# Kernel tuning notes

Hardware: AMD Instinct MI355X
Metric: run time of the kernel (lower is better)

## Reference

```python
import jax, jax.numpy as jnp
import numpy as np
from jax import lax

RADIUS = 2
DILATION = 2

def _mind_kernels():
    # 6-neighbourhood offsets within a 3x3x3 stencil
    six = np.array([[0, 1, 1], [1, 1, 0], [1, 0, 1], [1, 1, 2], [2, 1, 1], [1, 2, 1]], dtype=np.int64)
    # pairwise squared distances between the 6 offsets
    dist = ((six[:, None, :] - six[None, :, :]) ** 2).sum(-1)  # [6,6]
    i, j = np.meshgrid(np.arange(6), np.arange(6), indexing='ij')
    mask = ((i > j) & (dist == 2)).ravel()  # 12 True entries
    idx1 = six[np.repeat(np.arange(6), 6)][mask]  # [12,3]
    idx2 = six[np.tile(np.arange(6), 6)][mask]    # [12,3]
    m1 = np.zeros((12, 1, 3, 3, 3), np.float32)
    m2 = np.zeros((12, 1, 3, 3, 3), np.float32)
    m1[np.arange(12), 0, idx1[:, 0], idx1[:, 1], idx1[:, 2]] = 1.0
    m2[np.arange(12), 0, idx2[:, 0], idx2[:, 1], idx2[:, 2]] = 1.0
    return jnp.asarray(m1), jnp.asarray(m2)

MSHIFT1, MSHIFT2 = _mind_kernels()

def _rep_pad(x, p):
    # ReplicationPad3d on NCDHW
    return jnp.pad(x, ((0, 0), (0, 0), (p, p), (p, p), (p, p)), mode='edge')

def _shift_conv(x, w):
    # Conv3d(1->12, k=3, stride=1, padding=1, dilation=DILATION, bias=False)
    return lax.conv_general_dilated(
        x, w, window_strides=(1, 1, 1),
        padding=((1, 1), (1, 1), (1, 1)),
        rhs_dilation=(DILATION, DILATION, DILATION),
        dimension_numbers=('NCDHW', 'OIDHW', 'NCDHW'))

def _avg_pool3d(x, k):
    s = lax.reduce_window(x, jnp.float32(0.0), lax.add,
                          (1, 1, k, k, k), (1, 1, 1, 1, 1), 'VALID')
    return s / jnp.float32(k ** 3)

def mind3d(x):
    xp = _rep_pad(x, DILATION)
    diff = _shift_conv(xp, MSHIFT1) - _shift_conv(xp, MSHIFT2)  # [B,12,D+2,H+2,W+2]
    ssd = _avg_pool3d(_rep_pad(diff * diff, RADIUS), 2 * RADIUS + 1)
    mind = ssd - jnp.min(ssd, axis=1, keepdims=True)
    mind_var = jnp.mean(mind, axis=1, keepdims=True)  # [B,1,...]
    mv_mean = jnp.mean(mind_var)
    mind_var = jnp.clip(mind_var, mv_mean * 0.001, mv_mean * 1000.0)
    return jnp.exp(-mind / mind_var)

def setup_inputs() -> dict:
    key = jax.random.key(0)
    x = jax.random.uniform(key, (1, 1, 128, 128, 128), dtype=jnp.float32)
    return {"x": x}

def reference(x):
    return mind3d(x)
```

## Files before the change

kernel.cpp:

```cpp
#include <hip/hip_runtime.h>
#include <math.h>

#define N    130
#define NN   (130*130)
#define NNN  (130*130*130)
#define NQ4  (NNN/4)
#define NCH  12
#define XN   128
#define XNN  (XN*XN)

#define WT   11
#define HT   11
#define DSEGS 13
#define NWG  (WT*HT*DSEGS)

typedef float f32x4 __attribute__((ext_vector_type(4)));

template <int CTRL>
__device__ __forceinline__ float dppf(float v) {
    return __int_as_float(__builtin_amdgcn_update_dpp(
        0, __float_as_int(v), CTRL, 0xF, 0xF, true));
}
#define W5(v) ((v) + dppf<0x111>(v) + dppf<0x112>(v) \
                   + dppf<0x101>(v) + dppf<0x102>(v))

__global__ __launch_bounds__(256) void k_fused(const float* __restrict__ x,
                                               float* __restrict__ Cout,
                                               float* __restrict__ MV,
                                               double* __restrict__ acc,
                                               unsigned* __restrict__ gmm) {
    const int tid = threadIdx.x;
    const int wl  = tid & 15;
    const int r   = tid >> 4;

    const int qq  = NWG >> 3, rm = NWG & 7;
    const int xcd = blockIdx.x & 7, idx = blockIdx.x >> 3;
    const int b   = (xcd < rm ? xcd * (qq + 1)
                              : rm * (qq + 1) + (xcd - rm) * qq) + idx;

    const int wt   = b % WT;
    const int rest = b / WT;
    const int ht   = rest % HT;
    const int ds   = rest / HT;

    const int W0 = wt * 12;
    const int H0 = ht * 12;
    const int D0 = ds * 10;

    const int  w_gl = W0 + wl - 2;
    const int  bw   = min(max(w_gl, 0), 129);
    const int  ghW  = min(max(H0 - 2 + r, 0), 129);
    const int  oh   = H0 + r - 2;
    const bool interior = (r >= 2) && (r < 14);
    const bool validw   = (wl >= 2) && (wl < 14) && (w_gl < N);
    const bool valid    = interior && (oh < N) && validw;

    const int   ih_c = min(max(ghW - 1, 0), 127);
    const float fhm  = (ghW >= 1)   ? 1.0f : 0.0f;
    const float fhp  = (ghW <= 128) ? 1.0f : 0.0f;
    const int   dhm  = (min(max(ghW - 3, 0), 127) - ih_c) * XN;
    const int   dhp  = (min(ghW + 1, 127)        - ih_c) * XN;

    const int   col_c = ih_c * XN + min(max(bw - 1, 0), 127);
    const int   col_m = ih_c * XN + min(max(bw - 3, 0), 127);
    const int   col_p = ih_c * XN + min(bw + 1, 127);
    const float fw_m  = (bw >= 1)   ? 1.0f : 0.0f;
    const float fw_p  = (bw <= 128) ? 1.0f : 0.0f;

    __shared__ f32x4 Wlds[2][3][16][16];
    __shared__ float red[256];

    f32x4 ring[5][3];
    float lsum  = 0.0f;
    float mn_mv = INFINITY, mx_mv = 0.0f;
    int   voxoff = D0 * NN + oh * N + (valid ? w_gl : 0);

    float PF, fdpP;

#define PRE(IT) do {                                                          \
    const int dcn = min(max(D0 - 2 + (IT), 0), 129);                          \
    PF   = x[(size_t)(min(dcn + 1, 127)) * XNN + col_c];                      \
    fdpP = (dcn <= 128) ? 1.0f : 0.0f;                                        \
} while (0)

#define STEP(IT, SLOT, DOUT) do {                                             \
    const int it_ = (IT);                                                     \
    const int dc  = min(max(D0 - 2 + it_, 0), 129);                           \
    const float* pc = x + (size_t)(min(max(dc - 1, 0), 127)) * XNN;           \
    const float* pm = x + (size_t)(min(max(dc - 3, 0), 127)) * XNN;           \
    const float fdm = (dc >= 1) ? 1.0f : 0.0f;                                \
    const float y1 = PF * fdpP;                    \
    PRE(it_ + 1);                             \
    const float y0 = pm[col_c]       * fdm;                                   \
    const float y2 = pc[col_c + dhm] * fhm;                                   \
    const float y3 = pc[col_c + dhp] * fhp;                                   \
    const float y4 = pc[col_m]       * fw_m;                                  \
    const float y5 = pc[col_p]       * fw_p;                                  \
    float Wa[12];                                                             \
    { float t;                                                                \
      t = y4 - y0; Wa[0]  = t * t;  t = y2 - y0; Wa[1]  = t * t;              \
      t = y2 - y4; Wa[2]  = t * t;  t = y5 - y0; Wa[3]  = t * t;              \
      t = y5 - y2; Wa[4]  = t * t;  t = y1 - y4; Wa[5]  = t * t;              \
      t = y1 - y2; Wa[6]  = t * t;  t = y1 - y5; Wa[7]  = t * t;              \
      t = y3 - y0; Wa[8]  = t * t;  t = y3 - y4; Wa[9]  = t * t;              \
      t = y3 - y5; Wa[10] = t * t;  t = y3 - y1; Wa[11] = t * t; }            \
    _Pragma("unroll") for (int z = 0; z < 12; ++z) Wa[z] = W5(Wa[z]);         \
    const int pb = it_ & 1;                                                   \
    Wlds[pb][0][r][wl] = (f32x4){Wa[0], Wa[1], Wa[2],  Wa[3]};                \
    Wlds[pb][1][r][wl] = (f32x4){Wa[4], Wa[5], Wa[6],  Wa[7]};                \
    Wlds[pb][2][r][wl] = (f32x4){Wa[8], Wa[9], Wa[10], Wa[11]};               \
       \
    asm volatile("s_waitcnt lgkmcnt(0)" ::: "memory");                        \
    __builtin_amdgcn_s_barrier();                                             \
    if (interior) {                                                           \
        _Pragma("unroll") for (int g = 0; g < 3; ++g) {                       \
            f32x4 a = Wlds[pb][g][r - 2][wl];                                 \
            a += Wlds[pb][g][r - 1][wl];                                      \
            a += Wlds[pb][g][r    ][wl];                                      \
            a += Wlds[pb][g][r + 1][wl];                                      \
            a += Wlds[pb][g][r + 2][wl];                                      \
            ring[SLOT][g] = a;                                                \
        }                                                                     \
        if (DOUT) {                                                           \
            f32x4 sg[3];                                                      \
            _Pragma("unroll") for (int g = 0; g < 3; ++g) {                   \
                f32x4 a = ring[0][g];                                         \
                a += ring[1][g]; a += ring[2][g];                             \
                a += ring[3][g]; a += ring[4][g];                             \
                sg[g] = a * (1.0f / 125.0f);                                  \
            }                                                                 \
            float sv[12];                                                     \
            _Pragma("unroll") for (int g = 0; g < 3; ++g) {                   \
                sv[4*g+0] = sg[g].x; sv[4*g+1] = sg[g].y;                     \
                sv[4*g+2] = sg[g].z; sv[4*g+3] = sg[g].w;                     \
            }                                                                 \
            float mn = sv[0], tt = sv[0];                                     \
            _Pragma("unroll") for (int z = 1; z < 12; ++z) {                  \
                mn = fminf(mn, sv[z]); tt += sv[z];                           \
            }                                                                 \
            if (valid) {                                                      \
                const float mvar = tt * (1.0f / 12.0f) - mn;                  \
                const float inv  = 1.0f / fmaxf(mvar, 1e-20f);                \
                _Pragma("unroll") for (int z = 0; z < 12; ++z)                \
                    Cout[(size_t)z * NNN + (unsigned)voxoff] =                \
                        __expf(-(sv[z] - mn) * inv);                          \
                MV[(unsigned)voxoff] = mvar;                                  \
                lsum += mvar;                                                 \
                mn_mv = fminf(mn_mv, mvar);                                   \
                mx_mv = fmaxf(mx_mv, mvar);                                   \
                voxoff += NN;                                                 \
            }                                                                 \
        }                                                                     \
    }                                                                         \
} while (0)

    PRE(0);
    STEP(0, 0, false);
    STEP(1, 1, false);
    STEP(2, 2, false);
    STEP(3, 3, false);
    STEP(4, 4, true);  STEP(5, 0, true);  STEP(6, 1, true);
    STEP(7, 2, true);  STEP(8, 3, true);
    STEP(9, 4, true);  STEP(10, 0, true); STEP(11, 1, true);
    STEP(12, 2, true); STEP(13, 3, true);
#undef STEP
#undef PRE

    red[tid] = lsum;
    __syncthreads();
    for (int st = 128; st > 0; st >>= 1) {
        if (tid < st) red[tid] += red[tid + st];
        __syncthreads();
    }
    if (tid == 0) atomicAdd(acc, (double)red[0]);
    __syncthreads();
    red[tid] = mn_mv;
    __syncthreads();
    for (int st = 128; st > 0; st >>= 1) {
        if (tid < st) red[tid] = fminf(red[tid], red[tid + st]);
        __syncthreads();
    }
    if (tid == 0) atomicMin(&gmm[0], __float_as_uint(red[0]));
    __syncthreads();
    red[tid] = mx_mv;
    __syncthreads();
    for (int st = 128; st > 0; st >>= 1) {
        if (tid < st) red[tid] = fmaxf(red[tid], red[tid + st]);
        __syncthreads();
    }
    if (tid == 0) atomicMax(&gmm[1], __float_as_uint(red[0]));
}

__global__ void k_zero(double* acc, unsigned* gmm) {
    if (blockIdx.x == 0 && threadIdx.x == 0) {
        *acc = 0.0;
        gmm[0] = 0xFFFFFFFFu;
        gmm[1] = 0u;
    }
}

__global__ __launch_bounds__(256) void k_fix(float* __restrict__ io,
                                             const float* __restrict__ MV,
                                             const double* __restrict__ acc,
                                             const unsigned* __restrict__ gmm) {
    const float mv_mean = (float)(*acc * (1.0 / (double)NNN));
    const float lo = mv_mean * 0.001f, hi = mv_mean * 1000.0f;
    const float gmin = __uint_as_float(gmm[0]);
    const float gmax = __uint_as_float(gmm[1]);
    if (gmin >= lo && gmax <= hi) return;
    for (int q = blockIdx.x * 256 + threadIdx.x; q < NQ4;
         q += gridDim.x * 256) {
        const f32x4 mv = *((const f32x4*)MV + q);
        #pragma unroll
        for (int k = 0; k < 4; ++k) {
            const float used = fmaxf(mv[k], 1e-20f);
            const float cl   = fminf(fmaxf(mv[k], lo), hi);
            const float e    = used / cl;
            if (fabsf(e - 1.0f) > 1e-6f) {
                const size_t vox = (size_t)q * 4 + k;
                #pragma unroll
                for (int o = 0; o < NCH; ++o) {
                    const float v = io[(size_t)o * NNN + vox];
                    if (v > 0.0f)
                        io[(size_t)o * NNN + vox] = __powf(v, e);
                }
            }
        }
    }
}

extern "C" void kernel_launch(void* const* d_in, const int* in_sizes, int n_in,
                              void* d_out, int out_size, void* d_ws, size_t ws_size,
                              hipStream_t stream) {
    const float* x = (const float*)d_in[0];
    float* out = (float*)d_out;
    float* MV  = (float*)d_ws;
    double*  acc = (double*)((char*)d_ws + (size_t)NNN * sizeof(float));
    unsigned* gmm = (unsigned*)((char*)d_ws + (size_t)NNN * sizeof(float) + 8);

    k_zero <<<1, 64, 0, stream>>>(acc, gmm);
    k_fused<<<NWG, 256, 0, stream>>>(x, out, MV, acc, gmm);
    k_fix  <<<1024, 256, 0, stream>>>(out, MV, acc, gmm);
}
```

Measured before the change: 184.7 us.

## Replace LDS H-direction box sum with per-thread register recompute over five rows

The H-direction 5-tap sum no longer goes through double-buffered LDS with a barrier each depth step. Each thread now recomputes squared differences for five H rows from global memory and accumulates them in registers. Because all 16 rows are now outputs, the tile grows to 16 in H and 13 in depth, and the XCD-aware block remapping and the load prefetch are dropped. This removes the LDS traffic and per-step barriers at the cost of about five times more global loads and squared-difference arithmetic per step.

```diff
diff --git a/kernel.cpp b/kernel.cpp
--- a/kernel.cpp
+++ b/kernel.cpp
@@ -10,8 +10,8 @@
 #define XNN  (XN*XN)
 
 #define WT   11
-#define HT   11
-#define DSEGS 13
+#define HT   9
+#define DSEGS 10
 #define NWG  (WT*HT*DSEGS)
 
 typedef float f32x4 __attribute__((ext_vector_type(4)));
@@ -33,139 +33,122 @@
     const int wl  = tid & 15;
     const int r   = tid >> 4;
 
-    const int qq  = NWG >> 3, rm = NWG & 7;
-    const int xcd = blockIdx.x & 7, idx = blockIdx.x >> 3;
-    const int b   = (xcd < rm ? xcd * (qq + 1)
-                              : rm * (qq + 1) + (xcd - rm) * qq) + idx;
-
+    const int b    = blockIdx.x;
     const int wt   = b % WT;
     const int rest = b / WT;
     const int ht   = rest % HT;
     const int ds   = rest / HT;
 
     const int W0 = wt * 12;
-    const int H0 = ht * 12;
-    const int D0 = ds * 10;
+    const int H0 = ht * 16;
+    const int D0 = ds * 13;
 
     const int  w_gl = W0 + wl - 2;
     const int  bw   = min(max(w_gl, 0), 129);
-    const int  ghW  = min(max(H0 - 2 + r, 0), 129);
-    const int  oh   = H0 + r - 2;
-    const bool interior = (r >= 2) && (r < 14);
-    const bool validw   = (wl >= 2) && (wl < 14) && (w_gl < N);
-    const bool valid    = interior && (oh < N) && validw;
-
-    const int   ih_c = min(max(ghW - 1, 0), 127);
-    const float fhm  = (ghW >= 1)   ? 1.0f : 0.0f;
-    const float fhp  = (ghW <= 128) ? 1.0f : 0.0f;
-    const int   dhm  = (min(max(ghW - 3, 0), 127) - ih_c) * XN;
-    const int   dhp  = (min(ghW + 1, 127)        - ih_c) * XN;
-
-    const int   col_c = ih_c * XN + min(max(bw - 1, 0), 127);
-    const int   col_m = ih_c * XN + min(max(bw - 3, 0), 127);
-    const int   col_p = ih_c * XN + min(bw + 1, 127);
-    const float fw_m  = (bw >= 1)   ? 1.0f : 0.0f;
-    const float fw_p  = (bw <= 128) ? 1.0f : 0.0f;
-
-    __shared__ f32x4 Wlds[2][3][16][16];
-    __shared__ float red[256];
+    const int  oh   = H0 + r;
+    const bool valid = (wl >= 2) && (wl < 14) && (w_gl < N) && (oh < N);
+
+    const int   iwc  = min(max(bw - 1, 0), 127);
+    const int   iwm  = min(max(bw - 3, 0), 127);
+    const int   iwp  = min(bw + 1, 127);
+    const float fw_m = (bw >= 1)   ? 1.0f : 0.0f;
+    const float fw_p = (bw <= 128) ? 1.0f : 0.0f;
+
+    int   oc[5], om[5], op[5], o4[5], o5[5];
+    float fhm[5], fhp[5];
+    #pragma unroll
+    for (int k = 0; k < 5; ++k) {
+        const int ch = min(max(oh - 2 + k, 0), 129);
+        const int rc = min(max(ch - 1, 0), 127);
+        const int rm = min(max(ch - 3, 0), 127);
+        const int rp = min(ch + 1, 127);
+        oc[k] = rc * XN + iwc;
+        om[k] = rm * XN + iwc;
+        op[k] = rp * XN + iwc;
+        o4[k] = rc * XN + iwm;
+        o5[k] = rc * XN + iwp;
+        fhm[k] = (ch >= 1)   ? 1.0f : 0.0f;
+        fhp[k] = (ch <= 128) ? 1.0f : 0.0f;
+    }
 
     f32x4 ring[5][3];
     float lsum  = 0.0f;
     float mn_mv = INFINITY, mx_mv = 0.0f;
     int   voxoff = D0 * NN + oh * N + (valid ? w_gl : 0);
 
-    float PF, fdpP;
-
-#define PRE(IT) do {                                                          \
-    const int dcn = min(max(D0 - 2 + (IT), 0), 129);                          \
-    PF   = x[(size_t)(min(dcn + 1, 127)) * XNN + col_c];                      \
-    fdpP = (dcn <= 128) ? 1.0f : 0.0f;                                        \
-} while (0)
-
 #define STEP(IT, SLOT, DOUT) do {                                             \
-    const int it_ = (IT);                                                     \
-    const int dc  = min(max(D0 - 2 + it_, 0), 129);                           \
+    const int dc  = min(max(D0 - 2 + (IT), 0), 129);                          \
     const float* pc = x + (size_t)(min(max(dc - 1, 0), 127)) * XNN;           \
     const float* pm = x + (size_t)(min(max(dc - 3, 0), 127)) * XNN;           \
-    const float fdm = (dc >= 1) ? 1.0f : 0.0f;                                \
-    const float y1 = PF * fdpP;                    \
-    PRE(it_ + 1);                             \
-    const float y0 = pm[col_c]       * fdm;                                   \
-    const float y2 = pc[col_c + dhm] * fhm;                                   \
-    const float y3 = pc[col_c + dhp] * fhp;                                   \
-    const float y4 = pc[col_m]       * fw_m;                                  \
-    const float y5 = pc[col_p]       * fw_p;                                  \
-    float Wa[12];                                                             \
-    { float t;                                                                \
-      t = y4 - y0; Wa[0]  = t * t;  t = y2 - y0; Wa[1]  = t * t;              \
-      t = y2 - y4; Wa[2]  = t * t;  t = y5 - y0; Wa[3]  = t * t;              \
-      t = y5 - y2; Wa[4]  = t * t;  t = y1 - y4; Wa[5]  = t * t;              \
-      t = y1 - y2; Wa[6]  = t * t;  t = y1 - y5; Wa[7]  = t * t;              \
-      t = y3 - y0; Wa[8]  = t * t;  t = y3 - y4; Wa[9]  = t * t;              \
-      t = y3 - y5; Wa[10] = t * t;  t = y3 - y1; Wa[11] = t * t; }            \
-    _Pragma("unroll") for (int z = 0; z < 12; ++z) Wa[z] = W5(Wa[z]);         \
-    const int pb = it_ & 1;                                                   \
-    Wlds[pb][0][r][wl] = (f32x4){Wa[0], Wa[1], Wa[2],  Wa[3]};                \
-    Wlds[pb][1][r][wl] = (f32x4){Wa[4], Wa[5], Wa[6],  Wa[7]};                \
-    Wlds[pb][2][r][wl] = (f32x4){Wa[8], Wa[9], Wa[10], Wa[11]};               \
-       \
-    asm volatile("s_waitcnt lgkmcnt(0)" ::: "memory");                        \
-    __builtin_amdgcn_s_barrier();                                             \
-    if (interior) {                                                           \
+    const float* pp = x + (size_t)(min(dc + 1, 127)) * XNN;                   \
+    const float fdm = (dc >= 1)   ? 1.0f : 0.0f;                              \
+    const float fdp = (dc <= 128) ? 1.0f : 0.0f;                              \
+    float HS[12];                                                             \
+    _Pragma("unroll") for (int z = 0; z < 12; ++z) HS[z] = 0.0f;              \
+    _Pragma("unroll") for (int k = 0; k < 5; ++k) {                           \
+        const float y0 = pm[oc[k]] * fdm;                                     \
+        const float y1 = pp[oc[k]] * fdp;                                     \
+        const float y2 = pc[om[k]] * fhm[k];                                  \
+        const float y3 = pc[op[k]] * fhp[k];                                  \
+        const float y4 = pc[o4[k]] * fw_m;                                    \
+        const float y5 = pc[o5[k]] * fw_p;                                    \
+        float t;                                                              \
+        t = y4 - y0; HS[0]  += t * t;  t = y2 - y0; HS[1]  += t * t;          \
+        t = y2 - y4; HS[2]  += t * t;  t = y5 - y0; HS[3]  += t * t;          \
+        t = y5 - y2; HS[4]  += t * t;  t = y1 - y4; HS[5]  += t * t;          \
+        t = y1 - y2; HS[6]  += t * t;  t = y1 - y5; HS[7]  += t * t;          \
+        t = y3 - y0; HS[8]  += t * t;  t = y3 - y4; HS[9]  += t * t;          \
+        t = y3 - y5; HS[10] += t * t;  t = y3 - y1; HS[11] += t * t;          \
+    }                                                                         \
+     \
+    _Pragma("unroll") for (int z = 0; z < 12; ++z) HS[z] = W5(HS[z]);         \
+    ring[SLOT][0] = (f32x4){HS[0], HS[1], HS[2],  HS[3]};                     \
+    ring[SLOT][1] = (f32x4){HS[4], HS[5], HS[6],  HS[7]};                     \
+    ring[SLOT][2] = (f32x4){HS[8], HS[9], HS[10], HS[11]};                    \
+    if (DOUT) {                                                               \
+        f32x4 sg[3];                                                          \
         _Pragma("unroll") for (int g = 0; g < 3; ++g) {                       \
-            f32x4 a = Wlds[pb][g][r - 2][wl];                                 \
-            a += Wlds[pb][g][r - 1][wl];                                      \
-            a += Wlds[pb][g][r    ][wl];                                      \
-            a += Wlds[pb][g][r + 1][wl];                                      \
-            a += Wlds[pb][g][r + 2][wl];                                      \
-            ring[SLOT][g] = a;                                                \
-        }                                                                     \
-        if (DOUT) {                                                           \
-            f32x4 sg[3];                                                      \
-            _Pragma("unroll") for (int g = 0; g < 3; ++g) {                   \
-                f32x4 a = ring[0][g];                                         \
-                a += ring[1][g]; a += ring[2][g];                             \
-                a += ring[3][g]; a += ring[4][g];                             \
-                sg[g] = a * (1.0f / 125.0f);                                  \
-            }                                                                 \
-            float sv[12];                                                     \
-            _Pragma("unroll") for (int g = 0; g < 3; ++g) {                   \
-                sv[4*g+0] = sg[g].x; sv[4*g+1] = sg[g].y;                     \
-                sv[4*g+2] = sg[g].z; sv[4*g+3] = sg[g].w;                     \
-            }                                                                 \
-            float mn = sv[0], tt = sv[0];                                     \
-            _Pragma("unroll") for (int z = 1; z < 12; ++z) {                  \
-                mn = fminf(mn, sv[z]); tt += sv[z];                           \
-            }                                                                 \
-            if (valid) {                                                      \
-                const float mvar = tt * (1.0f / 12.0f) - mn;                  \
-                const float inv  = 1.0f / fmaxf(mvar, 1e-20f);                \
-                _Pragma("unroll") for (int z = 0; z < 12; ++z)                \
-                    Cout[(size_t)z * NNN + (unsigned)voxoff] =                \
-                        __expf(-(sv[z] - mn) * inv);                          \
-                MV[(unsigned)voxoff] = mvar;                                  \
-                lsum += mvar;                                                 \
-                mn_mv = fminf(mn_mv, mvar);                                   \
-                mx_mv = fmaxf(mx_mv, mvar);                                   \
-                voxoff += NN;                                                 \
-            }                                                                 \
+            f32x4 a = ring[0][g];                                             \
+            a += ring[1][g]; a += ring[2][g];                                 \
+            a += ring[3][g]; a += ring[4][g];                                 \
+            sg[g] = a * (1.0f / 125.0f);                                      \
+        }                                                                     \
+        float sv[12];                                                         \
+        _Pragma("unroll") for (int g = 0; g < 3; ++g) {                       \
+            sv[4*g+0] = sg[g].x; sv[4*g+1] = sg[g].y;                         \
+            sv[4*g+2] = sg[g].z; sv[4*g+3] = sg[g].w;                         \
+        }                                                                     \
+        float mn = sv[0], tt = sv[0];                                         \
+        _Pragma("unroll") for (int z = 1; z < 12; ++z) {                      \
+            mn = fminf(mn, sv[z]); tt += sv[z];                               \
+        }                                                                     \
+        if (valid) {                                                          \
+            const float mvar = tt * (1.0f / 12.0f) - mn;                      \
+            const float inv  = 1.0f / fmaxf(mvar, 1e-20f);                    \
+            _Pragma("unroll") for (int z = 0; z < 12; ++z)                    \
+                Cout[(size_t)z * NNN + (unsigned)voxoff] =                    \
+                    __expf(-(sv[z] - mn) * inv);                              \
+            MV[(unsigned)voxoff] = mvar;                                      \
+            lsum += mvar;                                                     \
+            mn_mv = fminf(mn_mv, mvar);                                       \
+            mx_mv = fmaxf(mx_mv, mvar);                                       \
+            voxoff += NN;                                                     \
         }                                                                     \
     }                                                                         \
 } while (0)
 
-    PRE(0);
     STEP(0, 0, false);
     STEP(1, 1, false);
     STEP(2, 2, false);
     STEP(3, 3, false);
-    STEP(4, 4, true);  STEP(5, 0, true);  STEP(6, 1, true);
-    STEP(7, 2, true);  STEP(8, 3, true);
-    STEP(9, 4, true);  STEP(10, 0, true); STEP(11, 1, true);
-    STEP(12, 2, true); STEP(13, 3, true);
+    STEP(4, 4, true);   STEP(5, 0, true);   STEP(6, 1, true);
+    STEP(7, 2, true);   STEP(8, 3, true);
+    STEP(9, 4, true);   STEP(10, 0, true);  STEP(11, 1, true);
+    STEP(12, 2, true);  STEP(13, 3, true);
+    STEP(14, 4, true);  STEP(15, 0, true);  STEP(16, 1, true);
 #undef STEP
-#undef PRE
-
+
+    __shared__ float red[256];
     red[tid] = lsum;
     __syncthreads();
     for (int st = 128; st > 0; st >>= 1) {
```

Result: slower. 194.7 us (+5.4%).
